# Performance work log

Hardware: AMD Instinct MI355X
Metric: run time of the kernel (lower is better)

The kernel has to match this reference:

```python
import jax, jax.numpy as jnp
import numpy as np

HIDDEN = 2048
SEL = 512
RES = HIDDEN - SEL
YSZ = 2048
RANK = 64
EPS = 1e-5


def _layernorm(x, gamma, beta):
    mu = jnp.mean(x, axis=-1, keepdims=True)
    var = jnp.mean(jnp.square(x - mu), axis=-1, keepdims=True)
    return (x - mu) * jax.lax.rsqrt(var + EPS) * gamma + beta


def setup_inputs() -> dict:
    key = jax.random.key(0)
    ks = jax.random.split(key, 8)
    B, S = 4, 4096
    hidden_states = jax.random.normal(ks[0], (B, S, HIDDEN), dtype=jnp.float32)
    y = jax.random.normal(ks[1], (B, S, YSZ), dtype=jnp.float32)
    A = -jnp.ones((1, 1, SEL), dtype=jnp.float32) + 0.02 * jax.random.normal(ks[2], (1, 1, SEL), dtype=jnp.float32)
    W_w = jax.random.normal(ks[3], (HIDDEN, YSZ), dtype=jnp.float32) * (1.0 / np.sqrt(YSZ))
    dd_w = jax.random.normal(ks[4], (RANK, HIDDEN + YSZ), dtype=jnp.float32) * (1.0 / np.sqrt(HIDDEN + YSZ))
    du_w = jax.random.normal(ks[5], (SEL, RANK), dtype=jnp.float32) * (1.0 / np.sqrt(RANK))
    t = 0.001 + jax.random.uniform(ks[6], (SEL,), dtype=jnp.float32) * (0.1 - 0.001)
    du_b = jnp.log(jnp.expm1(t))
    sel_gamma = jnp.ones((SEL,), dtype=jnp.float32)
    sel_beta = jnp.zeros((SEL,), dtype=jnp.float32)
    res_gamma = jnp.ones((RES,), dtype=jnp.float32)
    res_beta = jnp.zeros((RES,), dtype=jnp.float32)
    return {"hidden_states": hidden_states, "y": y, "A": A, "W_w": W_w,
            "dd_w": dd_w, "du_w": du_w, "du_b": du_b,
            "sel_gamma": sel_gamma, "sel_beta": sel_beta,
            "res_gamma": res_gamma, "res_beta": res_beta}


def reference(hidden_states, y, A, W_w, dd_w, du_w, du_b,
              sel_gamma, sel_beta, res_gamma, res_beta):
    sel_h = hidden_states[..., :SEL]
    res_h = hidden_states[..., SEL:]
    # W(y) split
    wy = jnp.einsum('bsy,hy->bsh', y, W_w)
    sel_y, res_y = wy[..., :SEL], wy[..., SEL:]
    # split layernorm of hidden_states
    normed = jnp.concatenate([
        _layernorm(sel_h, sel_gamma, sel_beta),
        _layernorm(res_h, res_gamma, res_beta)], axis=-1)
    # low-rank delta path
    cat = jnp.concatenate([normed, y], axis=-1)  # [B,S,HIDDEN+YSZ]
    low = jnp.einsum('bsc,rc->bsr', cat, dd_w)   # [B,S,RANK]
    delta = jnp.einsum('bsr,dr->bsd', low, du_w) + du_b  # [B,S,SEL]
    delta = jax.nn.softplus(delta)
    A_neg = -jax.nn.softplus(A)                  # [1,1,SEL]
    A_bar = jnp.exp(delta * A_neg)
    B_bar = (A_bar - 1.0) / A_neg
    sel_out = A_bar * sel_h + B_bar * sel_y
    res_out = res_h + res_y
    return jnp.concatenate([sel_out, res_out], axis=-1)
```

## Files before the change

### kernel.cpp

```cpp
#include <hip/hip_runtime.h>
#include <hip/hip_bf16.h>
#include <stdint.h>

#define NTOK   16384
#define HID    2048
#define SELN   512
#define YSZn   2048
#define EPSf   1e-5f

typedef __bf16 bf16x8 __attribute__((ext_vector_type(8)));
typedef float f32x4 __attribute__((ext_vector_type(4)));

__device__ __forceinline__ unsigned short f2bf(float f) {
  unsigned u = __float_as_uint(f);
  u += 0x7fff + ((u >> 16) & 1);
  return (unsigned short)(u >> 16);
}
__device__ __forceinline__ float bf2f(unsigned short h) {
  return __uint_as_float(((unsigned)h) << 16);
}
__device__ __forceinline__ float softplus_f(float x) {
  return fmaxf(x, 0.f) + log1pf(expf(-fabsf(x)));
}

#define GLD16(gp, lp) __builtin_amdgcn_global_load_lds( \
    (const __attribute__((address_space(1))) void*)(gp), \
    (__attribute__((address_space(3))) void*)(lp), 16, 0, 0)
#define BAR()  __builtin_amdgcn_s_barrier()
#define PRIO1() __builtin_amdgcn_s_setprio(1)
#define PRIO0() __builtin_amdgcn_s_setprio(0)

#define CY (NTOK * HID / 8)
#define CW (HID * YSZn / 8)
#define CD (64 * (HID + YSZn) / 8)
__global__ __launch_bounds__(256) void k_convert(
    const float* __restrict__ y, const float* __restrict__ Ww,
    const float* __restrict__ ddw,
    unsigned short* __restrict__ ybf, unsigned short* __restrict__ wbf,
    unsigned short* __restrict__ dbf) {
  int64_t stride = (int64_t)gridDim.x * blockDim.x;
  for (int64_t i = (int64_t)blockIdx.x * blockDim.x + threadIdx.x;
       i < CY + CW + CD; i += stride) {
    const float* src; unsigned short* dst;
    if (i < CY)            { src = y   + i * 8;            dst = ybf + i * 8; }
    else if (i < CY + CW)  { int64_t j = i - CY;       src = Ww  + j * 8; dst = wbf + j * 8; }
    else                   { int64_t j = i - CY - CW;  src = ddw + j * 8; dst = dbf + j * 8; }
    float4 a = ((const float4*)src)[0];
    float4 b = ((const float4*)src)[1];
    union { unsigned short u[8]; uint4 q; } o;
    o.u[0]=f2bf(a.x); o.u[1]=f2bf(a.y); o.u[2]=f2bf(a.z); o.u[3]=f2bf(a.w);
    o.u[4]=f2bf(b.x); o.u[5]=f2bf(b.y); o.u[6]=f2bf(b.z); o.u[7]=f2bf(b.w);
    *(uint4*)dst = o.q;
  }
}

__global__ __launch_bounds__(512, 2) void k_gemm_wy(
    const unsigned short* __restrict__ Y,
    const unsigned short* __restrict__ W,
    const float* __restrict__ hidden,
    unsigned short* __restrict__ wysel,
    float* __restrict__ out) {
  __shared__ char lds[131072];
  int bid = blockIdx.x;
  int nt = bid & 7, mt = bid >> 3;
  int m0 = mt * 256, n0 = nt * 256;
  int tid = threadIdx.x;
  int l = tid & 63, w = tid >> 6;
  int wr = w >> 2, wc = w & 3;

  int rowS[2], colS[2];
  #pragma unroll
  for (int i = 0; i < 2; ++i) {
    int L  = i * 8192 + tid * 16;
    int rb = L >> 10;
    int b  = L & 1023;
    int rr = (b >> 6) & 15;
    int cb = (b & 63) ^ ((rr >> 3) << 5);
    rowS[i] = rb * 16 + rr;
    colS[i] = cb >> 1;
  }
  const unsigned short* aSrc0 = Y + (size_t)(m0 + rowS[0]) * HID + colS[0];
  const unsigned short* aSrc1 = Y + (size_t)(m0 + rowS[1]) * HID + colS[1];
  const unsigned short* bSrc0 = W + (size_t)(n0 + rowS[0]) * HID + colS[0];
  const unsigned short* bSrc1 = W + (size_t)(n0 + rowS[1]) * HID + colS[1];

  int inner = (((l & 15) * 64) + ((l >> 4) * 16)) ^ (((l >> 3) & 1) << 5);
  const char* ldsp = (const char*)lds;

  f32x4 acc[8][4] = {};

#define STAGE_A(kt, kh, bb) do { \
    GLD16(aSrc0 + (size_t)(kt) * 64 + (kh) * 32, lds + (bb) + (kh) * 16384 + w * 1024); \
    GLD16(aSrc1 + (size_t)(kt) * 64 + (kh) * 32, lds + (bb) + (kh) * 16384 + 8192 + w * 1024); \
  } while (0)
#define STAGE_B(kt, kh, bb) do { \
    GLD16(bSrc0 + (size_t)(kt) * 64 + (kh) * 32, lds + 65536 + (bb) + (kh) * 16384 + w * 1024); \
    GLD16(bSrc1 + (size_t)(kt) * 64 + (kh) * 32, lds + 65536 + (bb) + (kh) * 16384 + 8192 + w * 1024); \
  } while (0)

  auto rdA = [&](int cbase, int kk, int mg, bf16x8* af) {
    #pragma unroll
    for (int mi = 0; mi < 4; ++mi)
      af[mi] = *(const bf16x8*)(ldsp + cbase + kk * 16384 +
                                (mg * 8 + wr * 4 + mi) * 1024 + inner);
  };
  auto rdB = [&](int cbase, int kk, bf16x8* bv) {
    #pragma unroll
    for (int ni = 0; ni < 4; ++ni)
      bv[ni] = *(const bf16x8*)(ldsp + 65536 + cbase + kk * 16384 +
                                (wc * 4 + ni) * 1024 + inner);
  };

  STAGE_A(0, 0, 0); STAGE_B(0, 0, 0); STAGE_A(0, 1, 0); STAGE_B(0, 1, 0);
  asm volatile("s_waitcnt vmcnt(4)");
  BAR();

  int buf = 0;
  for (int kt = 0; kt < 32; ++kt) {
    int cb = buf * 32768;
    int sb = 32768 - cb;
    bool last = (kt == 31);
    bf16x8 af[4], bv[4];

    rdA(cb, 0, 0, af); rdB(cb, 0, bv);
    if (!last) STAGE_A(kt + 1, 0, sb);
    BAR();
    asm volatile("s_waitcnt lgkmcnt(0)");
    PRIO1();
    #pragma unroll
    for (int mi = 0; mi < 4; ++mi)
      #pragma unroll
      for (int ni = 0; ni < 4; ++ni)
        acc[mi][ni] = __builtin_amdgcn_mfma_f32_16x16x32_bf16(af[mi], bv[ni], acc[mi][ni], 0, 0, 0);
    PRIO0();
    BAR();

    rdA(cb, 0, 1, af);
    if (!last) STAGE_B(kt + 1, 0, sb);
    BAR();
    asm volatile("s_waitcnt lgkmcnt(0)");
    PRIO1();
    #pragma unroll
    for (int mi = 0; mi < 4; ++mi)
      #pragma unroll
      for (int ni = 0; ni < 4; ++ni)
        acc[4 + mi][ni] = __builtin_amdgcn_mfma_f32_16x16x32_bf16(af[mi], bv[ni], acc[4 + mi][ni], 0, 0, 0);
    PRIO0();
    if (last) asm volatile("s_waitcnt vmcnt(0)");
    else      asm volatile("s_waitcnt vmcnt(4)");
    BAR();

    rdA(cb, 1, 0, af); rdB(cb, 1, bv);
    if (!last) STAGE_A(kt + 1, 1, sb);
    BAR();
    asm volatile("s_waitcnt lgkmcnt(0)");
    PRIO1();
    #pragma unroll
    for (int mi = 0; mi < 4; ++mi)
      #pragma unroll
      for (int ni = 0; ni < 4; ++ni)
        acc[mi][ni] = __builtin_amdgcn_mfma_f32_16x16x32_bf16(af[mi], bv[ni], acc[mi][ni], 0, 0, 0);
    PRIO0();
    BAR();

    rdA(cb, 1, 1, af);
    if (!last) STAGE_B(kt + 1, 1, sb);
    BAR();
    asm volatile("s_waitcnt lgkmcnt(0)");
    PRIO1();
    #pragma unroll
    for (int mi = 0; mi < 4; ++mi)
      #pragma unroll
      for (int ni = 0; ni < 4; ++ni)
        acc[4 + mi][ni] = __builtin_amdgcn_mfma_f32_16x16x32_bf16(af[mi], bv[ni], acc[4 + mi][ni], 0, 0, 0);
    PRIO0();
    if (!last) asm volatile("s_waitcnt vmcnt(4)");
    BAR();

    buf ^= 1;
  }

  if (nt < 2) {
    #pragma unroll
    for (int mg = 0; mg < 2; ++mg)
      #pragma unroll
      for (int mi = 0; mi < 4; ++mi)
        #pragma unroll
        for (int ni = 0; ni < 4; ++ni) {
          int row = m0 + mg * 128 + wr * 64 + mi * 16 + ((l >> 4) * 4);
          int col = n0 + wc * 64 + ni * 16 + (l & 15);
          #pragma unroll
          for (int rg = 0; rg < 4; ++rg)
            wysel[(size_t)(row + rg) * SELN + col] = f2bf(acc[mg * 4 + mi][ni][rg]);
        }
  } else {
    #pragma unroll
    for (int mg = 0; mg < 2; ++mg)
      #pragma unroll
      for (int mi = 0; mi < 4; ++mi)
        #pragma unroll
        for (int ni = 0; ni < 4; ++ni) {
          int row = m0 + mg * 128 + wr * 64 + mi * 16 + ((l >> 4) * 4);
          int col = n0 + wc * 64 + ni * 16 + (l & 15);
          #pragma unroll
          for (int rg = 0; rg < 4; ++rg) {
            size_t idx = (size_t)(row + rg) * HID + col;
            out[idx] = hidden[idx] + acc[mg * 4 + mi][ni][rg];
          }
        }
  }
#undef STAGE_A
#undef STAGE_B
}

__global__ __launch_bounds__(256) void k_ln(
    const float* __restrict__ hidden,
    const float* __restrict__ sg, const float* __restrict__ sb,
    const float* __restrict__ rg, const float* __restrict__ rb,
    unsigned short* __restrict__ normed) {
  int tok = blockIdx.x, tid = threadIdx.x;
  const float* x = hidden + (size_t)tok * HID;
  float4 a = ((const float4*)x)[tid * 2];
  float4 b = ((const float4*)x)[tid * 2 + 1];
  float v[8] = {a.x, a.y, a.z, a.w, b.x, b.y, b.z, b.w};
  float s = 0.f, ss = 0.f;
  #pragma unroll
  for (int j = 0; j < 8; ++j) { s += v[j]; ss += v[j] * v[j]; }
  #pragma unroll
  for (int off = 32; off > 0; off >>= 1) {
    s  += __shfl_xor(s, off);
    ss += __shfl_xor(ss, off);
  }
  __shared__ float ps[4], pss[4];
  int w = tid >> 6;
  if ((tid & 63) == 0) { ps[w] = s; pss[w] = ss; }
  __syncthreads();
  float mu, rstd; const float* gam; const float* bet; int cb;
  if (tid < 64) {
    float S = ps[0], SS = pss[0];
    mu = S * (1.f / 512.f);
    rstd = rsqrtf(SS * (1.f / 512.f) - mu * mu + EPSf);
    gam = sg; bet = sb; cb = tid * 8;
  } else {
    float S = ps[1] + ps[2] + ps[3], SS = pss[1] + pss[2] + pss[3];
    mu = S * (1.f / 1536.f);
    rstd = rsqrtf(SS * (1.f / 1536.f) - mu * mu + EPSf);
    gam = rg; bet = rb; cb = tid * 8 - 512;
  }
  union { unsigned short u[8]; uint4 q; } o;
  #pragma unroll
  for (int j = 0; j < 8; ++j)
    o.u[j] = f2bf((v[j] - mu) * rstd * gam[cb + j] + bet[cb + j]);
  *(uint4*)&normed[(size_t)tok * HID + tid * 8] = o.q;
}

__global__ __launch_bounds__(256) void k_gemm_low(
    const unsigned short* __restrict__ normed,
    const unsigned short* __restrict__ ybf,
    const unsigned short* __restrict__ ddw,
    float* __restrict__ low) {
  __shared__ char lds[32768];
  int m0 = blockIdx.x * 64;
  int tid = threadIdx.x, w = tid >> 6, l = tid & 63;
  f32x4 acc[4] = {};

  int rowS[2], colS[2];
  #pragma unroll
  for (int i = 0; i < 2; ++i) {
    int L  = i * 4096 + tid * 16;
    int sbt = L >> 10;
    int b  = L & 1023;
    int rr = (b >> 6) & 15;
    rowS[i] = (sbt >> 1) * 16 + rr;
    colS[i] = (sbt & 1) * 32 + (((b & 63) ^ ((rr >> 3) << 5)) >> 1);
  }
  int inner = (((l & 15) * 64) + ((l >> 4) * 16)) ^ (((l >> 3) & 1) << 5);
  const char* ldsp = (const char*)lds;

  auto stage = [&](const unsigned short* As_, int kt, int bb) {
    int k0 = (kt & 31) * 64;
    GLD16(As_ + (size_t)(m0 + rowS[0]) * HID + k0 + colS[0], lds + bb + w * 1024);
    GLD16(As_ + (size_t)(m0 + rowS[1]) * HID + k0 + colS[1], lds + bb + 4096 + w * 1024);
    GLD16(ddw + (size_t)rowS[0] * 4096 + kt * 64 + colS[0], lds + bb + 8192 + w * 1024);
    GLD16(ddw + (size_t)rowS[1] * 4096 + kt * 64 + colS[1], lds + bb + 8192 + 4096 + w * 1024);
  };

  stage(normed, 0, 0);
  asm volatile("s_waitcnt vmcnt(0)");
  BAR();
  int buf = 0;
  for (int kt = 0; kt < 64; ++kt) {
    int cb = buf * 16384, sb = 16384 - cb;
    if (kt < 63) stage((kt + 1 < 32) ? normed : ybf, kt + 1, sb);
    bf16x8 af0 = *(const bf16x8*)(ldsp + cb + (w * 2 + 0) * 1024 + inner);
    bf16x8 af1 = *(const bf16x8*)(ldsp + cb + (w * 2 + 1) * 1024 + inner);
    #pragma unroll
    for (int ni = 0; ni < 4; ++ni) {
      bf16x8 b0 = *(const bf16x8*)(ldsp + cb + 8192 + (ni * 2 + 0) * 1024 + inner);
      acc[ni] = __builtin_amdgcn_mfma_f32_16x16x32_bf16(af0, b0, acc[ni], 0, 0, 0);
    }
    #pragma unroll
    for (int ni = 0; ni < 4; ++ni) {
      bf16x8 b1 = *(const bf16x8*)(ldsp + cb + 8192 + (ni * 2 + 1) * 1024 + inner);
      acc[ni] = __builtin_amdgcn_mfma_f32_16x16x32_bf16(af1, b1, acc[ni], 0, 0, 0);
    }
    if (kt < 63) asm volatile("s_waitcnt vmcnt(0)");
    BAR();
    buf ^= 1;
  }
  #pragma unroll
  for (int ni = 0; ni < 4; ++ni) {
    int row = m0 + w * 16 + ((l >> 4) * 4);
    int col = ni * 16 + (l & 15);
    #pragma unroll
    for (int rg = 0; rg < 4; ++rg)
      low[(size_t)(row + rg) * 64 + col] = acc[ni][rg];
  }
}

__global__ __launch_bounds__(512) void k_final(
    const float* __restrict__ hidden,
    const unsigned short* __restrict__ wysel,
    const float* __restrict__ low,
    const float* __restrict__ A,
    const float* __restrict__ duw,
    const float* __restrict__ dub,
    float* __restrict__ out) {
  __shared__ float slow[8][64];
  int t0 = blockIdx.x * 8;
  int tid = threadIdx.x;
  slow[tid >> 6][tid & 63] = low[(size_t)t0 * 64 + tid];
  __syncthreads();

  int d = tid;
  float aneg = -softplus_f(A[d]);
  float dubv = dub[d];
  float wrow[64];
  #pragma unroll
  for (int r4 = 0; r4 < 16; ++r4) {
    float4 t = *(const float4*)&duw[(size_t)d * 64 + r4 * 4];
    wrow[r4 * 4 + 0] = t.x; wrow[r4 * 4 + 1] = t.y;
    wrow[r4 * 4 + 2] = t.z; wrow[r4 * 4 + 3] = t.w;
  }
  #pragma unroll 1
  for (int tk = 0; tk < 8; ++tk) {
    float acc = dubv;
    #pragma unroll
    for (int r = 0; r < 64; ++r) acc += wrow[r] * slow[tk][r];
    float delta = softplus_f(acc);
    float abar = expf(delta * aneg);
    float bbar = (abar - 1.f) / aneg;
    size_t tokb = (size_t)(t0 + tk);
    float selh = hidden[tokb * HID + d];
    float sely = bf2f(wysel[tokb * SELN + d]);
    out[tokb * HID + d] = abar * selh + bbar * sely;
  }
}

extern "C" void kernel_launch(void* const* d_in, const int* in_sizes, int n_in,
                              void* d_out, int out_size, void* d_ws, size_t ws_size,
                              hipStream_t stream) {
  (void)in_sizes; (void)n_in; (void)out_size; (void)ws_size;
  const float* hidden = (const float*)d_in[0];
  const float* y      = (const float*)d_in[1];
  const float* A      = (const float*)d_in[2];
  const float* Ww     = (const float*)d_in[3];
  const float* ddw    = (const float*)d_in[4];
  const float* duw    = (const float*)d_in[5];
  const float* dub    = (const float*)d_in[6];
  const float* sg     = (const float*)d_in[7];
  const float* sb     = (const float*)d_in[8];
  const float* rg     = (const float*)d_in[9];
  const float* rb     = (const float*)d_in[10];
  float* out = (float*)d_out;
  char* ws = (char*)d_ws;
  unsigned short* ybf   = (unsigned short*)(ws);
  unsigned short* wbf   = (unsigned short*)(ws + 67108864);
  unsigned short* dbf   = (unsigned short*)(ws + 75497472);
  unsigned short* wysel = (unsigned short*)(ws + 76021760);
  unsigned short* nrm   = (unsigned short*)(ws + 92798976);
  float*          low   = (float*)(ws + 159907840);

  hipLaunchKernelGGL(k_convert,  dim3(2048),  dim3(256), 0, stream, y, Ww, ddw, ybf, wbf, dbf);
  hipLaunchKernelGGL(k_gemm_wy,  dim3(512),   dim3(512), 0, stream, ybf, wbf, hidden, wysel, out);
  hipLaunchKernelGGL(k_ln,       dim3(16384), dim3(256), 0, stream, hidden, sg, sb, rg, rb, nrm);
  hipLaunchKernelGGL(k_gemm_low, dim3(256),   dim3(256), 0, stream, nrm, ybf, dbf, low);
  hipLaunchKernelGGL(k_final,    dim3(2048),  dim3(512), 0, stream, hidden, wysel, low, A, duw, dub, out);
}
```

Measured before the change: 631.0 us.

## Split-K low-rank GEMM, triple-buffer its loads, merge wy GEMM phases

The low-rank projection GEMM is split along K into two halves (normed and y), which doubles the block count from 256 to 512 so more CUs are busy. Each block gets a three-stage LDS ring in place of the old double buffer with a full wait every iteration. The final kernel sums the two partial results. The wy GEMM now loads all 8 A fragments per k-half and runs 32 MFMAs per phase, halving barriers, but needs more registers, so its occupancy hint drops from 2 to 1 blocks per SM. The extra partial buffer costs some added memory traffic and workspace.

```diff
diff --git a/kernel.cpp b/kernel.cpp
--- a/kernel.cpp
+++ b/kernel.cpp
@@ -54,7 +54,7 @@
   }
 }
 
-__global__ __launch_bounds__(512, 2) void k_gemm_wy(
+__global__ __launch_bounds__(512, 1) void k_gemm_wy(
     const unsigned short* __restrict__ Y,
     const unsigned short* __restrict__ W,
     const float* __restrict__ hidden,
@@ -98,19 +98,6 @@
     GLD16(bSrc1 + (size_t)(kt) * 64 + (kh) * 32, lds + 65536 + (bb) + (kh) * 16384 + 8192 + w * 1024); \
   } while (0)
 
-  auto rdA = [&](int cbase, int kk, int mg, bf16x8* af) {
-    #pragma unroll
-    for (int mi = 0; mi < 4; ++mi)
-      af[mi] = *(const bf16x8*)(ldsp + cbase + kk * 16384 +
-                                (mg * 8 + wr * 4 + mi) * 1024 + inner);
-  };
-  auto rdB = [&](int cbase, int kk, bf16x8* bv) {
-    #pragma unroll
-    for (int ni = 0; ni < 4; ++ni)
-      bv[ni] = *(const bf16x8*)(ldsp + 65536 + cbase + kk * 16384 +
-                                (wc * 4 + ni) * 1024 + inner);
-  };
-
   STAGE_A(0, 0, 0); STAGE_B(0, 0, 0); STAGE_A(0, 1, 0); STAGE_B(0, 1, 0);
   asm volatile("s_waitcnt vmcnt(4)");
   BAR();
@@ -120,59 +107,43 @@
     int cb = buf * 32768;
     int sb = 32768 - cb;
     bool last = (kt == 31);
-    bf16x8 af[4], bv[4];
-
-    rdA(cb, 0, 0, af); rdB(cb, 0, bv);
-    if (!last) STAGE_A(kt + 1, 0, sb);
+    bf16x8 af[8], bv[4];
+
+    #pragma unroll
+    for (int mi = 0; mi < 8; ++mi)
+      af[mi] = *(const bf16x8*)(ldsp + cb + ((mi >> 2) * 8 + wr * 4 + (mi & 3)) * 1024 + inner);
+    #pragma unroll
+    for (int ni = 0; ni < 4; ++ni)
+      bv[ni] = *(const bf16x8*)(ldsp + 65536 + cb + (wc * 4 + ni) * 1024 + inner);
+    if (!last) { STAGE_A(kt + 1, 0, sb); STAGE_B(kt + 1, 0, sb); }
     BAR();
     asm volatile("s_waitcnt lgkmcnt(0)");
     PRIO1();
     #pragma unroll
-    for (int mi = 0; mi < 4; ++mi)
+    for (int mi = 0; mi < 8; ++mi)
       #pragma unroll
       for (int ni = 0; ni < 4; ++ni)
         acc[mi][ni] = __builtin_amdgcn_mfma_f32_16x16x32_bf16(af[mi], bv[ni], acc[mi][ni], 0, 0, 0);
     PRIO0();
-    BAR();
-
-    rdA(cb, 0, 1, af);
-    if (!last) STAGE_B(kt + 1, 0, sb);
+    if (last) asm volatile("s_waitcnt vmcnt(0)");
+    else      asm volatile("s_waitcnt vmcnt(4)");
+    BAR();
+
+    #pragma unroll
+    for (int mi = 0; mi < 8; ++mi)
+      af[mi] = *(const bf16x8*)(ldsp + cb + 16384 + ((mi >> 2) * 8 + wr * 4 + (mi & 3)) * 1024 + inner);
+    #pragma unroll
+    for (int ni = 0; ni < 4; ++ni)
+      bv[ni] = *(const bf16x8*)(ldsp + 65536 + cb + 16384 + (wc * 4 + ni) * 1024 + inner);
+    if (!last) { STAGE_A(kt + 1, 1, sb); STAGE_B(kt + 1, 1, sb); }
     BAR();
     asm volatile("s_waitcnt lgkmcnt(0)");
     PRIO1();
     #pragma unroll
-    for (int mi = 0; mi < 4; ++mi)
-      #pragma unroll
-      for (int ni = 0; ni < 4; ++ni)
-        acc[4 + mi][ni] = __builtin_amdgcn_mfma_f32_16x16x32_bf16(af[mi], bv[ni], acc[4 + mi][ni], 0, 0, 0);
-    PRIO0();
-    if (last) asm volatile("s_waitcnt vmcnt(0)");
-    else      asm volatile("s_waitcnt vmcnt(4)");
-    BAR();
-
-    rdA(cb, 1, 0, af); rdB(cb, 1, bv);
-    if (!last) STAGE_A(kt + 1, 1, sb);
-    BAR();
-    asm volatile("s_waitcnt lgkmcnt(0)");
-    PRIO1();
-    #pragma unroll
-    for (int mi = 0; mi < 4; ++mi)
+    for (int mi = 0; mi < 8; ++mi)
       #pragma unroll
       for (int ni = 0; ni < 4; ++ni)
         acc[mi][ni] = __builtin_amdgcn_mfma_f32_16x16x32_bf16(af[mi], bv[ni], acc[mi][ni], 0, 0, 0);
-    PRIO0();
-    BAR();
-
-    rdA(cb, 1, 1, af);
-    if (!last) STAGE_B(kt + 1, 1, sb);
-    BAR();
-    asm volatile("s_waitcnt lgkmcnt(0)");
-    PRIO1();
-    #pragma unroll
-    for (int mi = 0; mi < 4; ++mi)
-      #pragma unroll
-      for (int ni = 0; ni < 4; ++ni)
-        acc[4 + mi][ni] = __builtin_amdgcn_mfma_f32_16x16x32_bf16(af[mi], bv[ni], acc[4 + mi][ni], 0, 0, 0);
     PRIO0();
     if (!last) asm volatile("s_waitcnt vmcnt(4)");
     BAR();
@@ -258,9 +229,12 @@
     const unsigned short* __restrict__ normed,
     const unsigned short* __restrict__ ybf,
     const unsigned short* __restrict__ ddw,
-    float* __restrict__ low) {
-  __shared__ char lds[32768];
-  int m0 = blockIdx.x * 64;
+    float* __restrict__ low2) {
+  __shared__ char lds[49152];
+  int b = blockIdx.x;
+  int m0 = (b >> 1) * 64;
+  int kh = b & 1;
+  const unsigned short* Asrc = kh ? ybf : normed;
   int tid = threadIdx.x, w = tid >> 6, l = tid & 63;
   f32x4 acc[4] = {};
 
@@ -269,59 +243,58 @@
   for (int i = 0; i < 2; ++i) {
     int L  = i * 4096 + tid * 16;
     int sbt = L >> 10;
-    int b  = L & 1023;
-    int rr = (b >> 6) & 15;
+    int bb = L & 1023;
+    int rr = (bb >> 6) & 15;
     rowS[i] = (sbt >> 1) * 16 + rr;
-    colS[i] = (sbt & 1) * 32 + (((b & 63) ^ ((rr >> 3) << 5)) >> 1);
+    colS[i] = (sbt & 1) * 32 + (((bb & 63) ^ ((rr >> 3) << 5)) >> 1);
   }
   int inner = (((l & 15) * 64) + ((l >> 4) * 16)) ^ (((l >> 3) & 1) << 5);
   const char* ldsp = (const char*)lds;
 
-  auto stage = [&](const unsigned short* As_, int kt, int bb) {
-    int k0 = (kt & 31) * 64;
-    GLD16(As_ + (size_t)(m0 + rowS[0]) * HID + k0 + colS[0], lds + bb + w * 1024);
-    GLD16(As_ + (size_t)(m0 + rowS[1]) * HID + k0 + colS[1], lds + bb + 4096 + w * 1024);
-    GLD16(ddw + (size_t)rowS[0] * 4096 + kt * 64 + colS[0], lds + bb + 8192 + w * 1024);
-    GLD16(ddw + (size_t)rowS[1] * 4096 + kt * 64 + colS[1], lds + bb + 8192 + 4096 + w * 1024);
+  auto stage = [&](int kt) {
+    int bb = (kt % 3) * 16384;
+    GLD16(Asrc + (size_t)(m0 + rowS[0]) * HID + kt * 64 + colS[0], lds + bb + w * 1024);
+    GLD16(Asrc + (size_t)(m0 + rowS[1]) * HID + kt * 64 + colS[1], lds + bb + 4096 + w * 1024);
+    GLD16(ddw + (size_t)rowS[0] * 4096 + kh * 2048 + kt * 64 + colS[0], lds + bb + 8192 + w * 1024);
+    GLD16(ddw + (size_t)rowS[1] * 4096 + kh * 2048 + kt * 64 + colS[1], lds + bb + 8192 + 4096 + w * 1024);
   };
 
-  stage(normed, 0, 0);
-  asm volatile("s_waitcnt vmcnt(0)");
-  BAR();
-  int buf = 0;
-  for (int kt = 0; kt < 64; ++kt) {
-    int cb = buf * 16384, sb = 16384 - cb;
-    if (kt < 63) stage((kt + 1 < 32) ? normed : ybf, kt + 1, sb);
-    bf16x8 af0 = *(const bf16x8*)(ldsp + cb + (w * 2 + 0) * 1024 + inner);
-    bf16x8 af1 = *(const bf16x8*)(ldsp + cb + (w * 2 + 1) * 1024 + inner);
+  stage(0); stage(1);
+  for (int kt = 0; kt < 32; ++kt) {
+    if (kt < 31) asm volatile("s_waitcnt vmcnt(4)");
+    else         asm volatile("s_waitcnt vmcnt(0)");
+    BAR();
+    int cbase = (kt % 3) * 16384;
+    bf16x8 af0 = *(const bf16x8*)(ldsp + cbase + (w * 2 + 0) * 1024 + inner);
+    bf16x8 af1 = *(const bf16x8*)(ldsp + cbase + (w * 2 + 1) * 1024 + inner);
     #pragma unroll
     for (int ni = 0; ni < 4; ++ni) {
-      bf16x8 b0 = *(const bf16x8*)(ldsp + cb + 8192 + (ni * 2 + 0) * 1024 + inner);
+      bf16x8 b0 = *(const bf16x8*)(ldsp + cbase + 8192 + (ni * 2 + 0) * 1024 + inner);
       acc[ni] = __builtin_amdgcn_mfma_f32_16x16x32_bf16(af0, b0, acc[ni], 0, 0, 0);
     }
     #pragma unroll
     for (int ni = 0; ni < 4; ++ni) {
-      bf16x8 b1 = *(const bf16x8*)(ldsp + cb + 8192 + (ni * 2 + 1) * 1024 + inner);
+      bf16x8 b1 = *(const bf16x8*)(ldsp + cbase + 8192 + (ni * 2 + 1) * 1024 + inner);
       acc[ni] = __builtin_amdgcn_mfma_f32_16x16x32_bf16(af1, b1, acc[ni], 0, 0, 0);
     }
-    if (kt < 63) asm volatile("s_waitcnt vmcnt(0)");
-    BAR();
-    buf ^= 1;
-  }
+    BAR();
+    if (kt + 2 < 32) stage(kt + 2);
+  }
+  float* dst = low2 + (size_t)kh * NTOK * 64;
   #pragma unroll
   for (int ni = 0; ni < 4; ++ni) {
     int row = m0 + w * 16 + ((l >> 4) * 4);
     int col = ni * 16 + (l & 15);
     #pragma unroll
     for (int rg = 0; rg < 4; ++rg)
-      low[(size_t)(row + rg) * 64 + col] = acc[ni][rg];
+      dst[(size_t)(row + rg) * 64 + col] = acc[ni][rg];
   }
 }
 
 __global__ __launch_bounds__(512) void k_final(
     const float* __restrict__ hidden,
     const unsigned short* __restrict__ wysel,
-    const float* __restrict__ low,
+    const float* __restrict__ low2,
     const float* __restrict__ A,
     const float* __restrict__ duw,
     const float* __restrict__ dub,
@@ -329,7 +302,10 @@
   __shared__ float slow[8][64];
   int t0 = blockIdx.x * 8;
   int tid = threadIdx.x;
-  slow[tid >> 6][tid & 63] = low[(size_t)t0 * 64 + tid];
+  {
+    size_t idx = (size_t)t0 * 64 + tid;
+    slow[tid >> 6][tid & 63] = low2[idx] + low2[(size_t)NTOK * 64 + idx];
+  }
   __syncthreads();
 
   int d = tid;
@@ -379,11 +355,11 @@
   unsigned short* dbf   = (unsigned short*)(ws + 75497472);
   unsigned short* wysel = (unsigned short*)(ws + 76021760);
   unsigned short* nrm   = (unsigned short*)(ws + 92798976);
-  float*          low   = (float*)(ws + 159907840);
+  float*          low2  = (float*)(ws + 159907840);
 
   hipLaunchKernelGGL(k_convert,  dim3(2048),  dim3(256), 0, stream, y, Ww, ddw, ybf, wbf, dbf);
   hipLaunchKernelGGL(k_gemm_wy,  dim3(512),   dim3(512), 0, stream, ybf, wbf, hidden, wysel, out);
   hipLaunchKernelGGL(k_ln,       dim3(16384), dim3(256), 0, stream, hidden, sg, sb, rg, rb, nrm);
-  hipLaunchKernelGGL(k_gemm_low, dim3(256),   dim3(256), 0, stream, nrm, ybf, dbf, low);
-  hipLaunchKernelGGL(k_final,    dim3(2048),  dim3(512), 0, stream, hidden, wysel, low, A, duw, dub, out);
-}
+  hipLaunchKernelGGL(k_gemm_low, dim3(512),   dim3(256), 0, stream, nrm, ybf, dbf, low2);
+  hipLaunchKernelGGL(k_final,    dim3(2048),  dim3(512), 0, stream, hidden, wysel, low2, A, duw, dub, out);
+}
```

After: 596.8 us. -5.4%, faster.
